# Kernel optimization log

Measured on AMD Instinct MI355X. Metric: run time of the kernel, lower is better.

The kernel has to match this reference:

```python
import jax, jax.numpy as jnp
import numpy as np

EMBED_DIM = 1024
NUM_HEADS = 16


def setup_inputs() -> dict:
    key = jax.random.key(0)
    k_x, k_w, k_b, k_ow, k_ob = jax.random.split(key, 5)
    B, S, E = 4, 2048, EMBED_DIM
    scale = 1.0 / np.sqrt(E)
    x = jax.random.normal(k_x, (B, S, E), dtype=jnp.float32)
    # nn.MultiheadAttention packed in-projection [3E, E] and out projection [E, E]
    in_proj_w = jax.random.uniform(k_w, (3 * E, E), dtype=jnp.float32, minval=-scale, maxval=scale)
    in_proj_b = jnp.zeros((3 * E,), dtype=jnp.float32)
    out_proj_w = jax.random.uniform(k_ow, (E, E), dtype=jnp.float32, minval=-scale, maxval=scale)
    out_proj_b = jnp.zeros((E,), dtype=jnp.float32)
    return {"x": x, "in_proj_w": in_proj_w, "in_proj_b": in_proj_b,
            "out_proj_w": out_proj_w, "out_proj_b": out_proj_b}


def reference(x, in_proj_w, in_proj_b, out_proj_w, out_proj_b):
    B, S, E = x.shape
    H = NUM_HEADS
    hd = E // H
    # packed QKV projection: [B,S,3E]
    qkv = x @ in_proj_w.T + in_proj_b
    q, k, v = jnp.split(qkv, 3, axis=-1)
    # [B,S,E] -> [B,H,S,hd]
    def to_heads(t):
        return t.reshape(B, S, H, hd).transpose(0, 2, 1, 3)
    q, k, v = to_heads(q), to_heads(k), to_heads(v)
    scale = 1.0 / jnp.sqrt(jnp.asarray(hd, dtype=x.dtype))
    scores = jnp.einsum('bhqd,bhkd->bhqk', q * scale, k)  # [B,H,S,S]
    # causal mask: position i attends to <= i (matches the -inf additive mask)
    causal = jnp.tril(jnp.ones((S, S), dtype=bool))
    scores = jnp.where(causal[None, None, :, :], scores, jnp.finfo(x.dtype).min)
    attn = jax.nn.softmax(scores, axis=-1)
    out = jnp.einsum('bhqk,bhkd->bhqd', attn, v)  # [B,H,S,hd]
    out = out.transpose(0, 2, 1, 3).reshape(B, S, E)
    return out @ out_proj_w.T + out_proj_b
```

## Files before the change

kernel.cpp:

```cpp
#include <hip/hip_runtime.h>
#include <stdint.h>

typedef _Float16 f16;
typedef _Float16 f16x2 __attribute__((ext_vector_type(2)));
typedef _Float16 f16x8 __attribute__((ext_vector_type(8)));
typedef float f32x4 __attribute__((ext_vector_type(4)));
typedef float f32x16 __attribute__((ext_vector_type(16)));
typedef uint32_t u32x4 __attribute__((ext_vector_type(4)));

#define B_   4
#define S_   2048
#define E_   1024
#define H_   16
#define HD_  64
#define BH_  (B_ * H_)

template <int N> struct IC { static constexpr int v = N; };

__device__ __forceinline__ void async_lds16(const void* g, void* l) {
    __builtin_amdgcn_global_load_lds(
        (__attribute__((address_space(1))) void*)(uintptr_t)g,
        (__attribute__((address_space(3))) void*)(uint32_t)(uintptr_t)l,
        16, 0, 0);
}

__global__ __launch_bounds__(256)
void cvt3(const float* __restrict__ x, const float* __restrict__ w1,
          const float* __restrict__ w2, f16* __restrict__ xb,
          f16* __restrict__ w1b, f16* __restrict__ w2b)
{
    const long i = (long)blockIdx.x * 256 + threadIdx.x;
    const float* src; f16* dst; long j;
    if (i < 1048576)      { src = x;  dst = xb;  j = i; }
    else if (i < 1441792) { src = w1; dst = w1b; j = i - 1048576; }
    else                  { src = w2; dst = w2b; j = i - 1441792; }
    const float4* p = (const float4*)src;
    float4 a = p[2 * j], b = p[2 * j + 1];
    f16x8 o;
    o[0] = (f16)a.x; o[1] = (f16)a.y; o[2] = (f16)a.z; o[3] = (f16)a.w;
    o[4] = (f16)b.x; o[5] = (f16)b.y; o[6] = (f16)b.z; o[7] = (f16)b.w;
    *(f16x8*)(dst + 8 * j) = o;
}

template <int MODE>
__global__ __launch_bounds__(512)
void gemm_pipe(const f16* __restrict__ A, const f16* __restrict__ Bm,
               const float* __restrict__ bias,
               f16* __restrict__ qo, f16* __restrict__ ko, f16* __restrict__ vto,
               float* __restrict__ Cf)
{
    constexpr int K = 1024, NT = 16;
    constexpr int N = (MODE == 0) ? 3072 : 1024;
    constexpr int NTN = N / 256;
    constexpr int NBLK = 64 * NTN;
    __shared__ __align__(16) f16 L[3][(128 + 256) * 64];
    const int tid = threadIdx.x, wave = tid >> 6, lane = tid & 63;
    const int lo = lane & 15, hi = lane >> 4;
    const int bid0 = blockIdx.x;
    const int bid = (bid0 & 7) * (NBLK / 8) + (bid0 >> 3);
    const int tm = bid / NTN, tn = bid % NTN;
    const long bm0 = (long)tm * 128, bn0 = (long)tn * 256;
    const int wr = (wave >> 2) * 64, wc = (wave & 3) * 64;

#define STAGE6(BUF, T)  do {                                                      \
    const long kk = (long)(T) * 64;                                               \
    _Pragma("unroll")                                                             \
    for (int j = 0; j < 2; ++j) {                                                 \
        const int c = j * 512 + tid;                                              \
        const int row = c >> 3, ch = c & 7;                                       \
        async_lds16(A + (bm0 + row) * K + kk + ((ch ^ (row & 7)) * 8),            \
                    &L[BUF][(j * 512 + wave * 64) * 8]);                          \
    }                                                                             \
    _Pragma("unroll")                                                             \
    for (int j = 0; j < 4; ++j) {                                                 \
        const int c = j * 512 + tid;                                              \
        const int row = c >> 3, ch = c & 7;                                       \
        async_lds16(Bm + (bn0 + row) * K + kk + ((ch ^ (row & 7)) * 8),           \
                    &L[BUF][8192 + (j * 512 + wave * 64) * 8]);                   \
    } } while (0)

    f32x4 acc[4][4] = {};

    auto tile = [&](auto bufc, int t) {
        constexpr int BUF = decltype(bufc)::v;
        constexpr int SBUF = (BUF + 2) % 3;
        if (t + 2 < NT) STAGE6(SBUF, t + 2);
        f16x8 af[2][4], bf[2][4];
#pragma unroll
        for (int kh = 0; kh < 2; ++kh) {
#pragma unroll
            for (int mi = 0; mi < 4; ++mi) {
                const int r = wr + mi * 16 + lo;
                af[kh][mi] = *(const f16x8*)&L[BUF][(r * 8 + ((kh * 4 + hi) ^ (r & 7))) * 8];
            }
#pragma unroll
            for (int ni = 0; ni < 4; ++ni) {
                const int r = wc + ni * 16 + lo;
                bf[kh][ni] = *(const f16x8*)&L[BUF][8192 + (r * 8 + ((kh * 4 + hi) ^ (r & 7))) * 8];
            }
        }
        __builtin_amdgcn_s_setprio(1);
#pragma unroll
        for (int kh = 0; kh < 2; ++kh)
#pragma unroll
            for (int mi = 0; mi < 4; ++mi)
#pragma unroll
                for (int ni = 0; ni < 4; ++ni)
                    acc[mi][ni] = __builtin_amdgcn_mfma_f32_16x16x32_f16(
                        af[kh][mi], bf[kh][ni], acc[mi][ni], 0, 0, 0);
        __builtin_amdgcn_s_setprio(0);
        if (t + 2 < NT) asm volatile("s_waitcnt vmcnt(6)" ::: "memory");
        else            asm volatile("s_waitcnt vmcnt(0)" ::: "memory");
        __builtin_amdgcn_sched_barrier(0);
        __builtin_amdgcn_s_barrier();
    };

    STAGE6(0, 0);
    STAGE6(1, 1);
    asm volatile("s_waitcnt vmcnt(6)" ::: "memory");
    __builtin_amdgcn_sched_barrier(0);
    __builtin_amdgcn_s_barrier();
    for (int t = 0; t < 15; t += 3) {
        tile(IC<0>{}, t);
        tile(IC<1>{}, t + 1);
        tile(IC<2>{}, t + 2);
    }
    tile(IC<0>{}, 15);
#undef STAGE6

    if (MODE == 1) {
#pragma unroll
        for (int mi = 0; mi < 4; ++mi)
#pragma unroll
            for (int ni = 0; ni < 4; ++ni)
#pragma unroll
                for (int j = 0; j < 4; ++j) {
                    const long r  = bm0 + wr + mi * 16 + 4 * hi + j;
                    const int  cn = (int)bn0 + wc + ni * 16 + lo;
                    Cf[r * N + cn] = acc[mi][ni][j] + bias[cn];
                }
        return;
    }

    const int which = (int)(bn0 >> 10);
    if (which < 2) {
#pragma unroll
        for (int mi = 0; mi < 4; ++mi)
#pragma unroll
            for (int ni = 0; ni < 4; ++ni)
#pragma unroll
                for (int j = 0; j < 4; ++j) {
                    const long r  = bm0 + wr + mi * 16 + 4 * hi + j;
                    const int  cn = (int)bn0 + wc + ni * 16 + lo;
                    const int  e = cn & 1023, h = e >> 6, d = e & 63;
                    const int  b = (int)(r >> 11), s = (int)(r & 2047);
                    const long bh = (long)b * H_ + h;
                    const f16 hv = (f16)(acc[mi][ni][j] + bias[cn]);
                    if (which == 0) qo[(bh * S_ + s) * HD_ + d] = hv;
                    else            ko[(bh * S_ + s) * HD_ + d] = hv;
                }
    } else {
        f16* T = ((f16*)L) + wave * 4096;
#pragma unroll
        for (int ni = 0; ni < 4; ++ni) {
            const int dl = ni * 16 + lo;
            const int dx = dl & 7;
#pragma unroll
            for (int mi = 0; mi < 4; ++mi)
#pragma unroll
                for (int j = 0; j < 4; ++j) {
                    const int sl = mi * 16 + 4 * hi + j;
                    const int cn = (int)bn0 + wc + ni * 16 + lo;
                    T[dl * 64 + ((((sl >> 3) ^ dx) << 3) | (sl & 7))] =
                        (f16)(acc[mi][ni][j] + bias[cn]);
                }
        }
        const int b = (int)(bm0 >> 11);
        const int sbase = (int)(bm0 & 2047) + wr;
        const int h = ((int)(bn0 & 1023) + wc) >> 6;
        const long vbase = (long)(b * H_ + h) * HD_;
#pragma unroll
        for (int it = 0; it < 8; ++it) {
            const int d = it * 8 + (lane >> 3);
            const int schunk = lane & 7;
            u32x4 val = *(const u32x4*)&T[d * 64 + ((schunk ^ (d & 7)) << 3)];
            *(u32x4*)&vto[(vbase + d) * S_ + sbase + schunk * 8] = val;
        }
    }
}

__global__ __launch_bounds__(512)
void attn_fwd(const f16* __restrict__ qb, const f16* __restrict__ kb,
              const f16* __restrict__ vtb, f16* __restrict__ ob)
{
    __shared__ __align__(16) f16 Ks[2][64 * 64];
    __shared__ __align__(16) f16 Vs[2][64 * 64];
    const int tid = threadIdx.x, wave = tid >> 6, lane = tid & 63;
    const int q32 = lane & 31, h2 = lane >> 5;
    const int bh = blockIdx.x;
    const int qtA = blockIdx.y;
    const int qtB = 15 - qtA;
    const int strip = (wave ^ (wave >> 2)) & 1;
    const int wrow  = wave >> 1;
    const int qw = (strip ? qtB : qtA) * 128 + wrow * 32;
    const long krow0 = (long)bh * S_;
    const long vrow0 = (long)bh * HD_;

#define STAGE(BUF, KV)  do {                                                      \
    async_lds16(kb  + (krow0 + (KV) + (tid & 63)) * HD_ + (tid >> 6) * 8,         \
                &Ks[BUF][wave * 512]);                                            \
    async_lds16(vtb + (vrow0 + (tid & 63)) * S_ + (KV) + (tid >> 6) * 8,          \
                &Vs[BUF][wave * 512]);                                            \
    } while (0)

    f16x8 qf[4];
    const f16 sch = (f16)0.1803368801f;
#pragma unroll
    for (int kkq = 0; kkq < 4; ++kkq) {
        qf[kkq] = *(const f16x8*)&qb[(krow0 + qw + q32) * HD_ + kkq * 16 + h2 * 8];
#pragma unroll
        for (int e = 0; e < 8; ++e) qf[kkq][e] *= sch;
    }

    f32x16 oacc[2] = {};
    float l_part = 0.f;
    const f16x2 ones2 = { (f16)1.0f, (f16)1.0f };
    const int qg = qw + q32;

    auto compute = [&](auto bufc, int t) {
        constexpr int BUF = decltype(bufc)::v;
        const int kv0 = t * 64;
        if (kv0 > qw + 31) return;

        f32x16 sc[2] = {};
        __builtin_amdgcn_s_setprio(1);
#pragma unroll
        for (int kkq = 0; kkq < 4; ++kkq)
#pragma unroll
            for (int ni = 0; ni < 2; ++ni) {
                f16x8 kf = *(const f16x8*)&Ks[BUF][(((kkq * 2 + h2) * 64) + ni * 32 + q32) * 8];
                sc[ni] = __builtin_amdgcn_mfma_f32_32x32x16_f16(kf, qf[kkq], sc[ni], 0, 0, 0);
            }
        __builtin_amdgcn_s_setprio(0);

        const bool maskp = (kv0 + 63) > qw;
#pragma unroll
        for (int ni = 0; ni < 2; ++ni)
#pragma unroll
            for (int r = 0; r < 16; ++r) {
                float p = __builtin_amdgcn_exp2f(sc[ni][r]);
                const int kvg = kv0 + ni * 32 + (r & 3) + 8 * (r >> 2) + 4 * h2;
                if (maskp && kvg > qg) p = 0.0f;
                sc[ni][r] = p;
            }

        __builtin_amdgcn_s_setprio(1);
#pragma unroll
        for (int ni = 0; ni < 2; ++ni) {
            uint32_t u[8];
#pragma unroll
            for (int m = 0; m < 8; ++m) {
                auto hp = __builtin_amdgcn_cvt_pkrtz(sc[ni][2 * m], sc[ni][2 * m + 1]);
                u[m] = __builtin_bit_cast(uint32_t, hp);
                l_part = __builtin_amdgcn_fdot2(__builtin_bit_cast(f16x2, u[m]), ones2, l_part, false);
            }
#pragma unroll
            for (int kkv = 0; kkv < 2; ++kkv) {
                auto sA = __builtin_amdgcn_permlane32_swap(u[4 * kkv + 0], u[4 * kkv + 2], false, false);
                auto sB = __builtin_amdgcn_permlane32_swap(u[4 * kkv + 1], u[4 * kkv + 3], false, false);
                u32x4 uv = { (uint32_t)sA[0], (uint32_t)sB[0], (uint32_t)sA[1], (uint32_t)sB[1] };
                f16x8 pf = __builtin_bit_cast(f16x8, uv);
                const int kg = ni * 2 + kkv;
#pragma unroll
                for (int dh = 0; dh < 2; ++dh) {
                    f16x8 vf = *(const f16x8*)&Vs[BUF][(((kg * 2 + h2) * 64) + dh * 32 + q32) * 8];
                    oacc[dh] = __builtin_amdgcn_mfma_f32_32x32x16_f16(pf, vf, oacc[dh], 0, 0, 0);
                }
            }
        }
        __builtin_amdgcn_s_setprio(0);
    };

    const int ntB = 2 * (qtB + 1);
    STAGE(0, 0);
    __syncthreads();
    for (int t = 0; t < ntB; t += 2) {
        STAGE(1, (t + 1) * 64);
        compute(IC<0>{}, t);
        __syncthreads();
        if (t + 2 < ntB) STAGE(0, (t + 2) * 64);
        compute(IC<1>{}, t + 1);
        __syncthreads();
    }
#undef STAGE

    const int b = bh >> 4, h = bh & 15;
    const float inv = 1.0f / (l_part + __shfl_xor(l_part, 32));
#pragma unroll
    for (int r = 0; r < 16; ++r) {
        const int crow = (r & 3) + 8 * (r >> 2) + 4 * h2;
        const float invr = __shfl(inv, crow);
#pragma unroll
        for (int dh = 0; dh < 2; ++dh)
            ob[((long)b * S_ + qw + crow) * E_ + h * HD_ + dh * 32 + q32] = (f16)(oacc[dh][r] * invr);
    }
}

extern "C" void kernel_launch(void* const* d_in, const int* in_sizes, int n_in,
                              void* d_out, int out_size, void* d_ws, size_t ws_size,
                              hipStream_t stream)
{
    (void)in_sizes; (void)n_in; (void)out_size; (void)ws_size;
    const float* x  = (const float*)d_in[0];
    const float* w1 = (const float*)d_in[1];
    const float* b1 = (const float*)d_in[2];
    const float* w2 = (const float*)d_in[3];
    const float* b2 = (const float*)d_in[4];
    float* out = (float*)d_out;

    char* ws = (char*)d_ws;
    f16* xb  = (f16*)ws;  ws += (size_t)8192 * 1024 * 2;
    f16* w1b = (f16*)ws;  ws += (size_t)3072 * 1024 * 2;
    f16* w2b = (f16*)ws;  ws += (size_t)1024 * 1024 * 2;
    f16* qb  = (f16*)ws;  ws += (size_t)BH_ * S_ * HD_ * 2;
    f16* kb  = (f16*)ws;  ws += (size_t)BH_ * S_ * HD_ * 2;
    f16* vtb = (f16*)ws;  ws += (size_t)BH_ * S_ * HD_ * 2;
    f16* ao  = (f16*)ws;  ws += (size_t)8192 * 1024 * 2;

    cvt3<<<dim3(6144), dim3(256), 0, stream>>>(x, w1, w2, xb, w1b, w2b);

    gemm_pipe<0><<<dim3(768), dim3(512), 0, stream>>>(xb, w1b, b1, qb, kb, vtb, nullptr);

    attn_fwd<<<dim3(64, 8), dim3(512), 0, stream>>>(qb, kb, vtb, ao);

    gemm_pipe<1><<<dim3(256), dim3(512), 0, stream>>>(ao, w2b, b2, nullptr, nullptr, nullptr, out);
}
```

Measured before the change: 159.5 us.

## Split paired causal attention blocks into single-tile 256-thread blocks

The attention kernel no longer packs a light and a heavy query tile into one 512-thread block. Each 256-thread block now handles one 128-row query tile, and blockIdx.y is remapped so that light and heavy tiles interleave across the grid. The old pairing forced the light half to wait while the heavy half looped over all KV tiles. The new layout doubles the number of blocks and leaves load balancing to the hardware scheduler, but each block now stages a K/V tile for only four waves, so there is less reuse per LDS load.

Result: no change. 160.0 us (+0.4%).

```diff
diff --git a/kernel.cpp b/kernel.cpp
--- a/kernel.cpp
+++ b/kernel.cpp
@@ -189,7 +189,7 @@
     }
 }
 
-__global__ __launch_bounds__(512)
+__global__ __launch_bounds__(256)
 void attn_fwd(const f16* __restrict__ qb, const f16* __restrict__ kb,
               const f16* __restrict__ vtb, f16* __restrict__ ob)
 {
@@ -198,20 +198,20 @@
     const int tid = threadIdx.x, wave = tid >> 6, lane = tid & 63;
     const int q32 = lane & 31, h2 = lane >> 5;
     const int bh = blockIdx.x;
-    const int qtA = blockIdx.y;
-    const int qtB = 15 - qtA;
-    const int strip = (wave ^ (wave >> 2)) & 1;
-    const int wrow  = wave >> 1;
-    const int qw = (strip ? qtB : qtA) * 128 + wrow * 32;
+    const int y = blockIdx.y, u = y >> 2, r4 = y & 3;
+    const int qt = (u & 1) ? (15 - 2 * r4 - (u >> 1)) : (2 * r4 + (u >> 1));
+    const int qw = qt * 128 + wave * 32;
     const long krow0 = (long)bh * S_;
     const long vrow0 = (long)bh * HD_;
 
 #define STAGE(BUF, KV)  do {                                                      \
-    async_lds16(kb  + (krow0 + (KV) + (tid & 63)) * HD_ + (tid >> 6) * 8,         \
-                &Ks[BUF][wave * 512]);                                            \
-    async_lds16(vtb + (vrow0 + (tid & 63)) * S_ + (KV) + (tid >> 6) * 8,          \
-                &Vs[BUF][wave * 512]);                                            \
-    } while (0)
+    _Pragma("unroll")                                                             \
+    for (int p = 0; p < 2; ++p) {                                                 \
+        const int n = p * 256 + tid;                                              \
+        const int base = (p * 256 + wave * 64) * 8;                               \
+        async_lds16(kb  + (krow0 + (KV) + (n & 63)) * HD_ + (n >> 6) * 8, &Ks[BUF][base]); \
+        async_lds16(vtb + (vrow0 + (n & 63)) * S_ + (KV) + (n >> 6) * 8, &Vs[BUF][base]);  \
+    } } while (0)
 
     f16x8 qf[4];
     const f16 sch = (f16)0.1803368801f;
@@ -257,17 +257,17 @@
         __builtin_amdgcn_s_setprio(1);
 #pragma unroll
         for (int ni = 0; ni < 2; ++ni) {
-            uint32_t u[8];
+            uint32_t u2[8];
 #pragma unroll
             for (int m = 0; m < 8; ++m) {
                 auto hp = __builtin_amdgcn_cvt_pkrtz(sc[ni][2 * m], sc[ni][2 * m + 1]);
-                u[m] = __builtin_bit_cast(uint32_t, hp);
-                l_part = __builtin_amdgcn_fdot2(__builtin_bit_cast(f16x2, u[m]), ones2, l_part, false);
+                u2[m] = __builtin_bit_cast(uint32_t, hp);
+                l_part = __builtin_amdgcn_fdot2(__builtin_bit_cast(f16x2, u2[m]), ones2, l_part, false);
             }
 #pragma unroll
             for (int kkv = 0; kkv < 2; ++kkv) {
-                auto sA = __builtin_amdgcn_permlane32_swap(u[4 * kkv + 0], u[4 * kkv + 2], false, false);
-                auto sB = __builtin_amdgcn_permlane32_swap(u[4 * kkv + 1], u[4 * kkv + 3], false, false);
+                auto sA = __builtin_amdgcn_permlane32_swap(u2[4 * kkv + 0], u2[4 * kkv + 2], false, false);
+                auto sB = __builtin_amdgcn_permlane32_swap(u2[4 * kkv + 1], u2[4 * kkv + 3], false, false);
                 u32x4 uv = { (uint32_t)sA[0], (uint32_t)sB[0], (uint32_t)sA[1], (uint32_t)sB[1] };
                 f16x8 pf = __builtin_bit_cast(f16x8, uv);
                 const int kg = ni * 2 + kkv;
@@ -281,14 +281,14 @@
         __builtin_amdgcn_s_setprio(0);
     };
 
-    const int ntB = 2 * (qtB + 1);
+    const int nt = 2 * (qt + 1);
     STAGE(0, 0);
     __syncthreads();
-    for (int t = 0; t < ntB; t += 2) {
+    for (int t = 0; t < nt; t += 2) {
         STAGE(1, (t + 1) * 64);
         compute(IC<0>{}, t);
         __syncthreads();
-        if (t + 2 < ntB) STAGE(0, (t + 2) * 64);
+        if (t + 2 < nt) STAGE(0, (t + 2) * 64);
         compute(IC<1>{}, t + 1);
         __syncthreads();
     }
@@ -331,7 +331,7 @@
 
     gemm_pipe<0><<<dim3(768), dim3(512), 0, stream>>>(xb, w1b, b1, qb, kb, vtb, nullptr);
 
-    attn_fwd<<<dim3(64, 8), dim3(512), 0, stream>>>(qb, kb, vtb, ao);
+    attn_fwd<<<dim3(64, 16), dim3(256), 0, stream>>>(qb, kb, vtb, ao);
 
     gemm_pipe<1><<<dim3(256), dim3(512), 0, stream>>>(ao, w2b, b2, nullptr, nullptr, nullptr, out);
 }
```
